# Optimization experiments

Measured on AMD Instinct MI355X. Metric: run time of the kernel, lower is better.

## Reference

```python
import jax, jax.numpy as jnp
import numpy as np

N_USERS = 100000
N_ITEMS = 50000
N_NODES = N_USERS + N_ITEMS
EMB_DIM = 64
N_EDGES = 4800000
N_LAYERS = 3


def setup_inputs() -> dict:
    key = jax.random.key(0)
    k1, k2, k3, k4, k5 = jax.random.split(key, 5)
    emb_user = jax.random.normal(k1, (N_USERS, EMB_DIM), dtype=jnp.float32) * 0.1
    emb_item = jax.random.normal(k2, (N_ITEMS, EMB_DIM), dtype=jnp.float32) * 0.1
    edge_row = jax.random.randint(k3, (N_EDGES,), 0, N_NODES, dtype=jnp.int32)
    edge_col = jax.random.randint(k4, (N_EDGES,), 0, N_NODES, dtype=jnp.int32)
    # normalized adjacency values (stand-in for 1/sqrt(d_i d_j))
    edge_val = jax.random.uniform(k5, (N_EDGES,), dtype=jnp.float32) * (1.0 / 32.0)
    return {"emb_user": emb_user, "emb_item": emb_item,
            "edge_row": edge_row, "edge_col": edge_col, "edge_val": edge_val}


def _spmm(edge_row, edge_col, edge_val, x, n_nodes):
    # COO SpMM: out[r] += val * x[c]
    msg = x[edge_col] * edge_val[:, None]          # [E, D]
    return jax.ops.segment_sum(msg, edge_row, num_segments=n_nodes)


def reference(emb_user, emb_item, edge_row, edge_col, edge_val):
    n_users = emb_user.shape[0]
    n_nodes = n_users + emb_item.shape[0]
    all_emb = jnp.concatenate([emb_user, emb_item], axis=0)  # [N, D]
    acc = all_emb
    cur = all_emb
    for _ in range(N_LAYERS):
        cur = _spmm(edge_row, edge_col, edge_val, cur, n_nodes)
        acc = acc + cur  # online accumulation instead of stack+mean
    light_out = acc / jnp.float32(N_LAYERS + 1)
    return light_out[:n_users], light_out[n_users:]
```

## Files before the change

kernel.cpp:

```cpp
#include <hip/hip_runtime.h>

#define N_USERS 100000
#define N_ITEMS 50000
#define N_NODES 150000
#define EMB_DIM 64
#define N_EDGES 4800000
#define N_LAYERS 3

#define NB 586
#define PA_BLOCK 512
#define PA_CHUNK_I4 2048

#define VAL_ENC (32.0f * 16383.0f)
#define VAL_DEC (1.0f / (32.0f * 16383.0f))

__device__ __forceinline__ ushort f2bf(float f) {
    unsigned int b = __float_as_uint(f);
    unsigned int r = (b + 0x7FFFu + ((b >> 16) & 1u)) >> 16;
    return (ushort)r;
}
__device__ __forceinline__ float bf2f(ushort u) {
    return __uint_as_float(((unsigned int)u) << 16);
}
__device__ __forceinline__ uint pack_cv(int c, float v) {
    uint vq = (uint)(v * VAL_ENC + 0.5f);
    if (vq > 16383u) vq = 16383u;
    return ((uint)c << 14) | vq;
}

__global__ void init_kernel(const float* __restrict__ emb_user,
                            const float* __restrict__ emb_item,
                            ushort* __restrict__ x0) {
    int i = blockIdx.x * blockDim.x + threadIdx.x;
    const int total = N_NODES * EMB_DIM / 4;
    if (i >= total) return;
    const int user_f4 = N_USERS * EMB_DIM / 4;
    float4 v;
    if (i < user_f4) v = reinterpret_cast<const float4*>(emb_user)[i];
    else             v = reinterpret_cast<const float4*>(emb_item)[i - user_f4];
    ushort4 h;
    h.x = f2bf(v.x); h.y = f2bf(v.y); h.z = f2bf(v.z); h.w = f2bf(v.w);
    reinterpret_cast<ushort4*>(x0)[i] = h;
}

__global__ void bucket_hist(const int* __restrict__ row, int* __restrict__ bucket_cnt) {
    __shared__ int cnt[NB];
    int t = threadIdx.x;
    for (int b = t; b < NB; b += 256) cnt[b] = 0;
    __syncthreads();
    int i = blockIdx.x * blockDim.x + t;
    int stride = gridDim.x * blockDim.x;
    for (int e = i; e < N_EDGES / 4; e += stride) {
        int4 r = reinterpret_cast<const int4*>(row)[e];
        atomicAdd(&cnt[r.x >> 8], 1);
        atomicAdd(&cnt[r.y >> 8], 1);
        atomicAdd(&cnt[r.z >> 8], 1);
        atomicAdd(&cnt[r.w >> 8], 1);
    }
    __syncthreads();
    for (int b = t; b < NB; b += 256) {
        int c = cnt[b];
        if (c) atomicAdd(&bucket_cnt[b], c);
    }
}

__global__ void bucket_scan(const int* __restrict__ bucket_cnt,
                            int* __restrict__ bucket_ptr,
                            int* __restrict__ bucket_cursor,
                            int* __restrict__ row_ptr) {
    __shared__ int lds[1024];
    int t = threadIdx.x;
    int v = (t < NB) ? bucket_cnt[t] : 0;
    lds[t] = v;
    __syncthreads();
    for (int off = 1; off < 1024; off <<= 1) {
        int x = (t >= off) ? lds[t - off] : 0;
        __syncthreads();
        lds[t] += x;
        __syncthreads();
    }
    int incl = lds[t];
    int excl = incl - v;
    if (t < NB) { bucket_ptr[t] = excl; bucket_cursor[t] = excl; }
    if (t == NB - 1) bucket_ptr[NB] = incl;
    if (t == 0) row_ptr[N_NODES] = N_EDGES;
}

__global__ void __launch_bounds__(PA_BLOCK)
pass_a(const int* __restrict__ row, const int* __restrict__ col,
       const float* __restrict__ val,
       int* __restrict__ bucket_cursor,
       uint2* __restrict__ tmp) {
    __shared__ int cnt[NB];
    __shared__ int cur[NB];
    int t = threadIdx.x;
    int start = blockIdx.x * PA_CHUNK_I4;
    int end = start + PA_CHUNK_I4;
    if (end > N_EDGES / 4) end = N_EDGES / 4;
    for (int b = t; b < NB; b += PA_BLOCK) cnt[b] = 0;
    __syncthreads();
    for (int i = start + t; i < end; i += PA_BLOCK) {
        int4 r = reinterpret_cast<const int4*>(row)[i];
        atomicAdd(&cnt[r.x >> 8], 1);
        atomicAdd(&cnt[r.y >> 8], 1);
        atomicAdd(&cnt[r.z >> 8], 1);
        atomicAdd(&cnt[r.w >> 8], 1);
    }
    __syncthreads();
    for (int b = t; b < NB; b += PA_BLOCK) {
        int c = cnt[b];
        cur[b] = c ? atomicAdd(&bucket_cursor[b], c) : 0;
    }
    __syncthreads();
    for (int i = start + t; i < end; i += PA_BLOCK) {
        int4 r = reinterpret_cast<const int4*>(row)[i];
        int4 c = reinterpret_cast<const int4*>(col)[i];
        float4 v = reinterpret_cast<const float4*>(val)[i];
        int p;
        p = atomicAdd(&cur[r.x >> 8], 1); tmp[p] = make_uint2(pack_cv(c.x, v.x), (uint)(r.x & 255));
        p = atomicAdd(&cur[r.y >> 8], 1); tmp[p] = make_uint2(pack_cv(c.y, v.y), (uint)(r.y & 255));
        p = atomicAdd(&cur[r.z >> 8], 1); tmp[p] = make_uint2(pack_cv(c.z, v.z), (uint)(r.z & 255));
        p = atomicAdd(&cur[r.w >> 8], 1); tmp[p] = make_uint2(pack_cv(c.w, v.w), (uint)(r.w & 255));
    }
}

__global__ void pass_b(const int* __restrict__ bucket_ptr,
                       const uint2* __restrict__ tmp,
                       int* __restrict__ row_ptr, uint* __restrict__ cv) {
    __shared__ int cnt[256];
    __shared__ int cur[256];
    __shared__ int wtot[4];
    int t = threadIdx.x;
    int b = blockIdx.x;
    int bp = bucket_ptr[b], be = bucket_ptr[b + 1];
    cnt[t] = 0;
    __syncthreads();
    for (int e = bp + t; e < be; e += 256) atomicAdd(&cnt[tmp[e].y], 1);
    __syncthreads();
    int v = cnt[t];
    int lane = t & 63, wv = t >> 6;
    int x = v;
    for (int off = 1; off < 64; off <<= 1) {
        int y = __shfl_up(x, off, 64);
        if (lane >= off) x += y;
    }
    if (lane == 63) wtot[wv] = x;
    __syncthreads();
    int woff = 0;
    for (int w = 0; w < wv; ++w) woff += wtot[w];
    int excl = x + woff - v;
    int gr = (b << 8) + t;
    if (gr < N_NODES) row_ptr[gr] = bp + excl;
    cur[t] = bp + excl;
    __syncthreads();
    for (int e = bp + t; e < be; e += 256) {
        uint2 rec = tmp[e];
        int pos = atomicAdd(&cur[rec.y], 1);
        cv[pos] = rec.x;
    }
}

template <int MODE>
__global__ void spmm_kernel(const int* __restrict__ row_ptr,
                            const uint* __restrict__ cvp,
                            const ushort* __restrict__ x,
                            ushort* __restrict__ y,
                            const float* __restrict__ emb_user,
                            const float* __restrict__ emb_item,
                            const ushort* __restrict__ y1,
                            const ushort* __restrict__ y2,
                            float* __restrict__ out) {
    int wave = threadIdx.x >> 6;
    int lane = threadIdx.x & 63;
    int r = blockIdx.x * 4 + wave;
    if (r >= N_NODES) return;
    int g = lane >> 4;
    int d = lane & 15;
    int s = row_ptr[r];
    int deg = row_ptr[r + 1] - s;
    const ushort4* xu = reinterpret_cast<const ushort4*>(x);
    float4 a4 = make_float4(0.f, 0.f, 0.f, 0.f);

    for (int base = 0; base < deg; base += 64) {
        int nload = deg - base;
        if (nload > 64) nload = 64;
        uint mycv = cvp[s + base + (lane < nload ? lane : nload - 1)];
        int rounds4 = (nload + 15) >> 4;
        for (int k4 = 0; k4 < rounds4; ++k4) {
            int i0 = (k4 << 4) + g;
            int i1 = i0 + 4, i2 = i0 + 8, i3 = i0 + 12;
            uint c0 = __shfl(mycv, i0, 64);
            uint c1 = __shfl(mycv, i1, 64);
            uint c2 = __shfl(mycv, i2, 64);
            uint c3 = __shfl(mycv, i3, 64);
            ushort4 xv0 = xu[((c0 >> 14) << 4) + d];
            ushort4 xv1 = xu[((c1 >> 14) << 4) + d];
            ushort4 xv2 = xu[((c2 >> 14) << 4) + d];
            ushort4 xv3 = xu[((c3 >> 14) << 4) + d];
            float v0 = (i0 < nload) ? (float)(c0 & 16383u) * VAL_DEC : 0.f;
            float v1 = (i1 < nload) ? (float)(c1 & 16383u) * VAL_DEC : 0.f;
            float v2 = (i2 < nload) ? (float)(c2 & 16383u) * VAL_DEC : 0.f;
            float v3 = (i3 < nload) ? (float)(c3 & 16383u) * VAL_DEC : 0.f;
            a4.x += v0 * bf2f(xv0.x); a4.y += v0 * bf2f(xv0.y);
            a4.z += v0 * bf2f(xv0.z); a4.w += v0 * bf2f(xv0.w);
            a4.x += v1 * bf2f(xv1.x); a4.y += v1 * bf2f(xv1.y);
            a4.z += v1 * bf2f(xv1.z); a4.w += v1 * bf2f(xv1.w);
            a4.x += v2 * bf2f(xv2.x); a4.y += v2 * bf2f(xv2.y);
            a4.z += v2 * bf2f(xv2.z); a4.w += v2 * bf2f(xv2.w);
            a4.x += v3 * bf2f(xv3.x); a4.y += v3 * bf2f(xv3.y);
            a4.z += v3 * bf2f(xv3.z); a4.w += v3 * bf2f(xv3.w);
        }
    }
    for (int off = 16; off <= 32; off <<= 1) {
        a4.x += __shfl_xor(a4.x, off, 64);
        a4.y += __shfl_xor(a4.y, off, 64);
        a4.z += __shfl_xor(a4.z, off, 64);
        a4.w += __shfl_xor(a4.w, off, 64);
    }
    if (g == 0) {
        int o = (r << 4) + d;
        if (MODE == 0) {
            ushort4 h;
            h.x = f2bf(a4.x); h.y = f2bf(a4.y); h.z = f2bf(a4.z); h.w = f2bf(a4.w);
            reinterpret_cast<ushort4*>(y)[o] = h;
        } else {
            const float4* eb = (r < N_USERS)
                ? reinterpret_cast<const float4*>(emb_user) + ((size_t)r << 4)
                : reinterpret_cast<const float4*>(emb_item) + ((size_t)(r - N_USERS) << 4);
            float4 ev = eb[d];
            ushort4 h1 = reinterpret_cast<const ushort4*>(y1)[o];
            ushort4 h2 = reinterpret_cast<const ushort4*>(y2)[o];
            float4 rr;
            rr.x = (ev.x + bf2f(h1.x) + bf2f(h2.x) + a4.x) * 0.25f;
            rr.y = (ev.y + bf2f(h1.y) + bf2f(h2.y) + a4.y) * 0.25f;
            rr.z = (ev.z + bf2f(h1.z) + bf2f(h2.z) + a4.z) * 0.25f;
            rr.w = (ev.w + bf2f(h1.w) + bf2f(h2.w) + a4.w) * 0.25f;
            reinterpret_cast<float4*>(out)[o] = rr;
        }
    }
}

__global__ void fb_init(const float* __restrict__ emb_user,
                        const float* __restrict__ emb_item,
                        float* __restrict__ cur, float* __restrict__ acc) {
    int i = blockIdx.x * blockDim.x + threadIdx.x;
    const int total = N_NODES * EMB_DIM / 4;
    if (i >= total) return;
    const int user_f4 = N_USERS * EMB_DIM / 4;
    float4 v;
    if (i < user_f4) v = reinterpret_cast<const float4*>(emb_user)[i];
    else             v = reinterpret_cast<const float4*>(emb_item)[i - user_f4];
    reinterpret_cast<float4*>(cur)[i] = v;
    reinterpret_cast<float4*>(acc)[i] = v;
}

__global__ void scatter_kernel(const int* __restrict__ edge_row,
                               const int* __restrict__ edge_col,
                               const float* __restrict__ edge_val,
                               const float* __restrict__ x,
                               float* __restrict__ y) {
    long long tid = (long long)blockIdx.x * blockDim.x + threadIdx.x;
    long long e = tid >> 4;
    int sub = (int)(tid & 15);
    if (e >= N_EDGES) return;
    int r = edge_row[e];
    int c = edge_col[e];
    float v = edge_val[e];
    float4 xv = reinterpret_cast<const float4*>(x)[(long long)c * 16 + sub];
    float* dst = y + ((long long)r * EMB_DIM + sub * 4);
    atomicAdd(dst + 0, v * xv.x);
    atomicAdd(dst + 1, v * xv.y);
    atomicAdd(dst + 2, v * xv.z);
    atomicAdd(dst + 3, v * xv.w);
}

template <bool FINAL>
__global__ void add_kernel(const float* __restrict__ nxt, float* __restrict__ acc) {
    int i = blockIdx.x * blockDim.x + threadIdx.x;
    const int total = N_NODES * EMB_DIM / 4;
    if (i >= total) return;
    float4 a = reinterpret_cast<float4*>(acc)[i];
    float4 b = reinterpret_cast<const float4*>(nxt)[i];
    a.x += b.x; a.y += b.y; a.z += b.z; a.w += b.w;
    if (FINAL) {
        const float s = 1.0f / (N_LAYERS + 1);
        a.x *= s; a.y *= s; a.z *= s; a.w *= s;
    }
    reinterpret_cast<float4*>(acc)[i] = a;
}

extern "C" void kernel_launch(void* const* d_in, const int* in_sizes, int n_in,
                              void* d_out, int out_size, void* d_ws, size_t ws_size,
                              hipStream_t stream) {
    const float* emb_user = (const float*)d_in[0];
    const float* emb_item = (const float*)d_in[1];
    const int*   edge_row = (const int*)d_in[2];
    const int*   edge_col = (const int*)d_in[3];
    const float* edge_val = (const float*)d_in[4];
    float* out = (float*)d_out;

    const size_t x_bytes = (size_t)N_NODES * EMB_DIM * sizeof(ushort);

    char* base = (char*)d_ws;
    uint*   cv = (uint*)base;
    ushort* x0 = (ushort*)(base + (size_t)N_EDGES * 4);
    ushort* x1 = (ushort*)((char*)x0 + x_bytes);
    ushort* x2 = (ushort*)((char*)x1 + x_bytes);
    char* meta = (char*)x2 + x_bytes;
    int* row_ptr       = (int*)meta;
    int* bucket_cnt    = row_ptr + N_NODES + 2;
    int* bucket_ptr    = bucket_cnt + NB;
    int* bucket_cursor = bucket_ptr + NB + 1;
    size_t need = (size_t)((char*)(bucket_cursor + NB) - base);
    uint2* tmp = (uint2*)x0;

    const int BT = 256;
    const int total_f4 = N_NODES * EMB_DIM / 4;
    const int grid_f4 = (total_f4 + BT - 1) / BT;

    if (ws_size >= need) {
        hipMemsetAsync(bucket_cnt, 0, NB * sizeof(int), stream);
        bucket_hist<<<512, BT, 0, stream>>>(edge_row, bucket_cnt);
        bucket_scan<<<1, 1024, 0, stream>>>(bucket_cnt, bucket_ptr, bucket_cursor, row_ptr);
        const int grid_a = (N_EDGES / 4 + PA_CHUNK_I4 - 1) / PA_CHUNK_I4;
        pass_a<<<grid_a, PA_BLOCK, 0, stream>>>(edge_row, edge_col, edge_val,
                                                bucket_cursor, tmp);
        pass_b<<<NB, BT, 0, stream>>>(bucket_ptr, tmp, row_ptr, cv);

        init_kernel<<<grid_f4, BT, 0, stream>>>(emb_user, emb_item, x0);
        const int grid_rows = (N_NODES + 3) / 4;
        spmm_kernel<0><<<grid_rows, BT, 0, stream>>>(row_ptr, cv, x0, x1,
                                                     nullptr, nullptr, nullptr, nullptr, nullptr);
        spmm_kernel<0><<<grid_rows, BT, 0, stream>>>(row_ptr, cv, x1, x2,
                                                     nullptr, nullptr, nullptr, nullptr, nullptr);
        spmm_kernel<1><<<grid_rows, BT, 0, stream>>>(row_ptr, cv, x2, nullptr,
                                                     emb_user, emb_item, x1, x2, out);
    } else {
        const size_t buf_elems = (size_t)N_NODES * EMB_DIM;
        const size_t buf_bytes = buf_elems * sizeof(float);
        float* bufA = (float*)d_ws;
        float* bufB = bufA + buf_elems;
        fb_init<<<grid_f4, BT, 0, stream>>>(emb_user, emb_item, bufA, out);
        const long long scatter_threads = (long long)N_EDGES * 16;
        const int grid_sc = (int)((scatter_threads + BT - 1) / BT);
        float* cur = bufA;
        float* nxt = bufB;
        for (int layer = 0; layer < N_LAYERS; ++layer) {
            hipMemsetAsync(nxt, 0, buf_bytes, stream);
            scatter_kernel<<<grid_sc, BT, 0, stream>>>(edge_row, edge_col, edge_val, cur, nxt);
            if (layer == N_LAYERS - 1) add_kernel<true><<<grid_f4, BT, 0, stream>>>(nxt, out);
            else                        add_kernel<false><<<grid_f4, BT, 0, stream>>>(nxt, out);
            float* t = cur; cur = nxt; nxt = t;
        }
    }
}
```

Baseline: 384.2 us.

## Fuse histogram into block-local LDS sort and gather per-bucket segments

Removes the separate global histogram pass by having pass_a count buckets, scan locally, sort its 8192-edge chunk into LDS, and write it contiguously with per-block bucket offsets. Pass_b then gathers each bucket's segments from all blocks into LDS and performs the row-level counting sort from LDS instead of global memory. This is meant to cut one full read of edge_row, the global atomic cursor contention, and the scattered writes of the old pass_a. In exchange it uses large LDS allocations (64KB rec buffers) that limit occupancy, and the fixed PB_CAP assumes bucket sizes stay bounded.

```diff
diff --git a/kernel.cpp b/kernel.cpp
--- a/kernel.cpp
+++ b/kernel.cpp
@@ -8,8 +8,10 @@
 #define N_LAYERS 3
 
 #define NB 586
-#define PA_BLOCK 512
-#define PA_CHUNK_I4 2048
+#define NBP1 (NB + 1)
+#define PA_EDGES 8192
+#define PA_BLOCKS ((N_EDGES + PA_EDGES - 1) / PA_EDGES)
+#define PB_CAP 9088
 
 #define VAL_ENC (32.0f * 16383.0f)
 #define VAL_DEC (1.0f / (32.0f * 16383.0f))
@@ -43,30 +45,73 @@
     reinterpret_cast<ushort4*>(x0)[i] = h;
 }
 
-__global__ void bucket_hist(const int* __restrict__ row, int* __restrict__ bucket_cnt) {
+__global__ void __launch_bounds__(512)
+pass_a(const int* __restrict__ row, const int* __restrict__ col,
+       const float* __restrict__ val,
+       int* __restrict__ bucket_cnt,
+       uint2* __restrict__ tmp, int* __restrict__ offs) {
+    __shared__ uint2 rec[PA_EDGES];
     __shared__ int cnt[NB];
+    __shared__ int cur[NB];
+    __shared__ int scan_tmp[512];
     int t = threadIdx.x;
-    for (int b = t; b < NB; b += 256) cnt[b] = 0;
-    __syncthreads();
-    int i = blockIdx.x * blockDim.x + t;
-    int stride = gridDim.x * blockDim.x;
-    for (int e = i; e < N_EDGES / 4; e += stride) {
-        int4 r = reinterpret_cast<const int4*>(row)[e];
+    int blk = blockIdx.x;
+    int e0 = blk * PA_EDGES;
+    int ecnt = N_EDGES - e0;
+    if (ecnt > PA_EDGES) ecnt = PA_EDGES;
+    int i4cnt = ecnt >> 2;
+    const int4*   rp = reinterpret_cast<const int4*>(row) + (e0 >> 2);
+    const int4*   cp = reinterpret_cast<const int4*>(col) + (e0 >> 2);
+    const float4* vp = reinterpret_cast<const float4*>(val) + (e0 >> 2);
+
+    for (int b = t; b < NB; b += 512) cnt[b] = 0;
+    __syncthreads();
+    for (int i = t; i < i4cnt; i += 512) {
+        int4 r = rp[i];
         atomicAdd(&cnt[r.x >> 8], 1);
         atomicAdd(&cnt[r.y >> 8], 1);
         atomicAdd(&cnt[r.z >> 8], 1);
         atomicAdd(&cnt[r.w >> 8], 1);
     }
     __syncthreads();
-    for (int b = t; b < NB; b += 256) {
+    for (int b = t; b < NB; b += 512) {
         int c = cnt[b];
         if (c) atomicAdd(&bucket_cnt[b], c);
     }
+    int i0 = 2 * t, i1 = 2 * t + 1;
+    int a0 = (i0 < NB) ? cnt[i0] : 0;
+    int a1 = (i1 < NB) ? cnt[i1] : 0;
+    scan_tmp[t] = a0 + a1;
+    __syncthreads();
+    for (int off = 1; off < 512; off <<= 1) {
+        int x = (t >= off) ? scan_tmp[t - off] : 0;
+        __syncthreads();
+        scan_tmp[t] += x;
+        __syncthreads();
+    }
+    int pair_excl = scan_tmp[t] - (a0 + a1);
+    int* offs_row = offs + (size_t)blk * NBP1;
+    if (i0 < NB) { cur[i0] = pair_excl;      offs_row[i0] = pair_excl; }
+    if (i1 < NB) { cur[i1] = pair_excl + a0; offs_row[i1] = pair_excl + a0; }
+    if (t == 0) offs_row[NB] = ecnt;
+    __syncthreads();
+    for (int i = t; i < i4cnt; i += 512) {
+        int4 r = rp[i];
+        int4 c = cp[i];
+        float4 v = vp[i];
+        int p;
+        p = atomicAdd(&cur[r.x >> 8], 1); rec[p] = make_uint2(pack_cv(c.x, v.x), (uint)(r.x & 255));
+        p = atomicAdd(&cur[r.y >> 8], 1); rec[p] = make_uint2(pack_cv(c.y, v.y), (uint)(r.y & 255));
+        p = atomicAdd(&cur[r.z >> 8], 1); rec[p] = make_uint2(pack_cv(c.z, v.z), (uint)(r.z & 255));
+        p = atomicAdd(&cur[r.w >> 8], 1); rec[p] = make_uint2(pack_cv(c.w, v.w), (uint)(r.w & 255));
+    }
+    __syncthreads();
+    uint2* dst = tmp + (size_t)blk * PA_EDGES;
+    for (int i = t; i < ecnt; i += 512) dst[i] = rec[i];
 }
 
 __global__ void bucket_scan(const int* __restrict__ bucket_cnt,
                             int* __restrict__ bucket_ptr,
-                            int* __restrict__ bucket_cursor,
                             int* __restrict__ row_ptr) {
     __shared__ int lds[1024];
     int t = threadIdx.x;
@@ -80,83 +125,68 @@
         __syncthreads();
     }
     int incl = lds[t];
-    int excl = incl - v;
-    if (t < NB) { bucket_ptr[t] = excl; bucket_cursor[t] = excl; }
+    if (t < NB) bucket_ptr[t] = incl - v;
     if (t == NB - 1) bucket_ptr[NB] = incl;
     if (t == 0) row_ptr[N_NODES] = N_EDGES;
 }
 
-__global__ void __launch_bounds__(PA_BLOCK)
-pass_a(const int* __restrict__ row, const int* __restrict__ col,
-       const float* __restrict__ val,
-       int* __restrict__ bucket_cursor,
-       uint2* __restrict__ tmp) {
-    __shared__ int cnt[NB];
-    __shared__ int cur[NB];
-    int t = threadIdx.x;
-    int start = blockIdx.x * PA_CHUNK_I4;
-    int end = start + PA_CHUNK_I4;
-    if (end > N_EDGES / 4) end = N_EDGES / 4;
-    for (int b = t; b < NB; b += PA_BLOCK) cnt[b] = 0;
-    __syncthreads();
-    for (int i = start + t; i < end; i += PA_BLOCK) {
-        int4 r = reinterpret_cast<const int4*>(row)[i];
-        atomicAdd(&cnt[r.x >> 8], 1);
-        atomicAdd(&cnt[r.y >> 8], 1);
-        atomicAdd(&cnt[r.z >> 8], 1);
-        atomicAdd(&cnt[r.w >> 8], 1);
-    }
-    __syncthreads();
-    for (int b = t; b < NB; b += PA_BLOCK) {
-        int c = cnt[b];
-        cur[b] = c ? atomicAdd(&bucket_cursor[b], c) : 0;
-    }
-    __syncthreads();
-    for (int i = start + t; i < end; i += PA_BLOCK) {
-        int4 r = reinterpret_cast<const int4*>(row)[i];
-        int4 c = reinterpret_cast<const int4*>(col)[i];
-        float4 v = reinterpret_cast<const float4*>(val)[i];
-        int p;
-        p = atomicAdd(&cur[r.x >> 8], 1); tmp[p] = make_uint2(pack_cv(c.x, v.x), (uint)(r.x & 255));
-        p = atomicAdd(&cur[r.y >> 8], 1); tmp[p] = make_uint2(pack_cv(c.y, v.y), (uint)(r.y & 255));
-        p = atomicAdd(&cur[r.z >> 8], 1); tmp[p] = make_uint2(pack_cv(c.z, v.z), (uint)(r.z & 255));
-        p = atomicAdd(&cur[r.w >> 8], 1); tmp[p] = make_uint2(pack_cv(c.w, v.w), (uint)(r.w & 255));
-    }
-}
-
-__global__ void pass_b(const int* __restrict__ bucket_ptr,
-                       const uint2* __restrict__ tmp,
-                       int* __restrict__ row_ptr, uint* __restrict__ cv) {
+__global__ void __launch_bounds__(512)
+pass_b(const int* __restrict__ bucket_ptr, const int* __restrict__ offs,
+       const uint2* __restrict__ tmp,
+       int* __restrict__ row_ptr, uint* __restrict__ cv) {
+    __shared__ uint2 rec[PB_CAP];
+    __shared__ int oa[PA_BLOCKS];
+    __shared__ int ob[PA_BLOCKS];
     __shared__ int cnt[256];
     __shared__ int cur[256];
     __shared__ int wtot[4];
+    __shared__ int lds_total;
     int t = threadIdx.x;
     int b = blockIdx.x;
-    int bp = bucket_ptr[b], be = bucket_ptr[b + 1];
-    cnt[t] = 0;
-    __syncthreads();
-    for (int e = bp + t; e < be; e += 256) atomicAdd(&cnt[tmp[e].y], 1);
-    __syncthreads();
-    int v = cnt[t];
     int lane = t & 63, wv = t >> 6;
+    if (t < 256) cnt[t] = 0;
+    if (t == 0) lds_total = 0;
+    for (int j = t; j < PA_BLOCKS; j += 512) {
+        oa[j] = offs[(size_t)j * NBP1 + b];
+        ob[j] = offs[(size_t)j * NBP1 + b + 1];
+    }
+    __syncthreads();
+    for (int j = wv; j < PA_BLOCKS; j += 8) {
+        int s = oa[j];
+        int n = ob[j] - s;
+        if (n <= 0) continue;
+        int base = 0;
+        if (lane == 0) base = atomicAdd(&lds_total, n);
+        base = __shfl(base, 0, 64);
+        const uint2* src = tmp + (size_t)j * PA_EDGES + s;
+        for (int k = lane; k < n; k += 64) rec[base + k] = src[k];
+    }
+    __syncthreads();
+    int total = lds_total;
+    for (int i = t; i < total; i += 512) atomicAdd(&cnt[rec[i].y], 1);
+    __syncthreads();
+    int v = (t < 256) ? cnt[t] : 0;
     int x = v;
     for (int off = 1; off < 64; off <<= 1) {
         int y = __shfl_up(x, off, 64);
         if (lane >= off) x += y;
     }
-    if (lane == 63) wtot[wv] = x;
-    __syncthreads();
-    int woff = 0;
-    for (int w = 0; w < wv; ++w) woff += wtot[w];
-    int excl = x + woff - v;
-    int gr = (b << 8) + t;
-    if (gr < N_NODES) row_ptr[gr] = bp + excl;
-    cur[t] = bp + excl;
-    __syncthreads();
-    for (int e = bp + t; e < be; e += 256) {
-        uint2 rec = tmp[e];
-        int pos = atomicAdd(&cur[rec.y], 1);
-        cv[pos] = rec.x;
+    if (t < 256 && lane == 63) wtot[wv] = x;
+    __syncthreads();
+    if (t < 256) {
+        int woff = 0;
+        for (int w = 0; w < wv; ++w) woff += wtot[w];
+        int excl = woff + x - v;
+        int base = bucket_ptr[b];
+        int gr = (b << 8) + t;
+        if (gr < N_NODES) row_ptr[gr] = base + excl;
+        cur[t] = base + excl;
+    }
+    __syncthreads();
+    for (int i = t; i < total; i += 512) {
+        uint2 r = rec[i];
+        int pos = atomicAdd(&cur[r.y], 1);
+        cv[pos] = r.x;
     }
 }
 
@@ -300,19 +330,20 @@
     float* out = (float*)d_out;
 
     const size_t x_bytes = (size_t)N_NODES * EMB_DIM * sizeof(ushort);
+    const size_t tmp_bytes = (size_t)PA_BLOCKS * PA_EDGES * sizeof(uint2);
 
     char* base = (char*)d_ws;
-    uint*   cv = (uint*)base;
-    ushort* x0 = (ushort*)(base + (size_t)N_EDGES * 4);
-    ushort* x1 = (ushort*)((char*)x0 + x_bytes);
-    ushort* x2 = (ushort*)((char*)x1 + x_bytes);
+    uint*  cv  = (uint*)base;
+    uint2* tmp = (uint2*)(base + (size_t)N_EDGES * 4);
+    int*   offs = (int*)((char*)tmp + tmp_bytes);
+    ushort* x2 = (ushort*)((char*)offs + (size_t)PA_BLOCKS * NBP1 * 4);
     char* meta = (char*)x2 + x_bytes;
-    int* row_ptr       = (int*)meta;
-    int* bucket_cnt    = row_ptr + N_NODES + 2;
-    int* bucket_ptr    = bucket_cnt + NB;
-    int* bucket_cursor = bucket_ptr + NB + 1;
-    size_t need = (size_t)((char*)(bucket_cursor + NB) - base);
-    uint2* tmp = (uint2*)x0;
+    int* row_ptr    = (int*)meta;
+    int* bucket_cnt = row_ptr + N_NODES + 2;
+    int* bucket_ptr = bucket_cnt + NB;
+    size_t need = (size_t)((char*)(bucket_ptr + NBP1) - base);
+    ushort* x0 = (ushort*)tmp;
+    ushort* x1 = (ushort*)((char*)tmp + x_bytes);
 
     const int BT = 256;
     const int total_f4 = N_NODES * EMB_DIM / 4;
@@ -320,12 +351,10 @@
 
     if (ws_size >= need) {
         hipMemsetAsync(bucket_cnt, 0, NB * sizeof(int), stream);
-        bucket_hist<<<512, BT, 0, stream>>>(edge_row, bucket_cnt);
-        bucket_scan<<<1, 1024, 0, stream>>>(bucket_cnt, bucket_ptr, bucket_cursor, row_ptr);
-        const int grid_a = (N_EDGES / 4 + PA_CHUNK_I4 - 1) / PA_CHUNK_I4;
-        pass_a<<<grid_a, PA_BLOCK, 0, stream>>>(edge_row, edge_col, edge_val,
-                                                bucket_cursor, tmp);
-        pass_b<<<NB, BT, 0, stream>>>(bucket_ptr, tmp, row_ptr, cv);
+        pass_a<<<PA_BLOCKS, 512, 0, stream>>>(edge_row, edge_col, edge_val,
+                                              bucket_cnt, tmp, offs);
+        bucket_scan<<<1, 1024, 0, stream>>>(bucket_cnt, bucket_ptr, row_ptr);
+        pass_b<<<NB, 512, 0, stream>>>(bucket_ptr, offs, tmp, row_ptr, cv);
 
         init_kernel<<<grid_f4, BT, 0, stream>>>(emb_user, emb_item, x0);
         const int grid_rows = (N_NODES + 3) / 4;
```

Result: slower. 450.3 us (+17.2%).
